# Kernel tuning notes

Hardware: AMD Instinct MI355X
Metric: run time of the kernel (lower is better)

The kernel has to match this reference:

```python
import jax, jax.numpy as jnp
import numpy as np

N = 262144  # num_channels (o*i)
K = 5       # kernel_size


def setup_inputs() -> dict:
    key = jax.random.key(0)
    k1, k2, k3 = jax.random.split(key, 3)
    return {
        "input_filter": jax.random.normal(k1, (N, K, K, K), dtype=jnp.float32),
        "theta_v": jax.random.normal(k2, (N, 3), dtype=jnp.float32),
        "theta": jax.random.normal(k3, (N,), dtype=jnp.float32),
    }


def _rodrigues(theta_v, theta):
    # F.normalize(theta_v, p=2) with eps=1e-12
    norm = jnp.linalg.norm(theta_v, axis=-1, keepdims=True)
    v = theta_v / jnp.maximum(norm, 1e-12)
    vx, vy, vz = v[:, 0], v[:, 1], v[:, 2]
    z = jnp.zeros_like(vx)
    # skew-symmetric cross-product matrix m, shape (n,3,3)
    m = jnp.stack([z, -vz, vy,
                   vz, z, -vx,
                   -vy, vx, z], axis=-1).reshape(-1, 3, 3)
    s = jnp.sin(theta)[:, None, None]
    c = (1.0 - jnp.cos(theta))[:, None, None]
    I3 = jnp.eye(3, dtype=theta_v.dtype)
    return I3 + s * m + c * jnp.einsum('nij,njk->nik', m, m)


def _base_grid(k):
    # matches _get_base_grids: coord along axis i -> channel 0, j -> 1, l -> 2
    c = jnp.linspace(-1.0, 1.0, k, dtype=jnp.float32)
    gi, gj, gl = jnp.meshgrid(c, c, c, indexing='ij')
    return jnp.stack([gi, gj, gl], axis=-1).reshape(k * k * k, 3)  # (k^3, 3)


def _grid_sample_3d_zeros(vol, grid):
    # vol: (n, D, H, W); grid: (n, P, 3) in [-1,1], channels (x->W, y->H, z->D)
    # trilinear, align_corners=True, padding_mode='zeros'
    n, D, H, W = vol.shape
    x = (grid[..., 0] + 1.0) * 0.5 * (W - 1)
    y = (grid[..., 1] + 1.0) * 0.5 * (H - 1)
    z = (grid[..., 2] + 1.0) * 0.5 * (D - 1)
    x0f, y0f, z0f = jnp.floor(x), jnp.floor(y), jnp.floor(z)
    wx, wy, wz = x - x0f, y - y0f, z - z0f
    x0, y0, z0 = x0f.astype(jnp.int32), y0f.astype(jnp.int32), z0f.astype(jnp.int32)
    bidx = jnp.arange(n)[:, None]
    out = jnp.zeros(grid.shape[:-1], dtype=vol.dtype)
    for dz in (0, 1):
        for dy in (0, 1):
            for dx in (0, 1):
                zi, yi, xi = z0 + dz, y0 + dy, x0 + dx
                w = ((wz if dz else 1.0 - wz) *
                     (wy if dy else 1.0 - wy) *
                     (wx if dx else 1.0 - wx))
                inb = ((zi >= 0) & (zi < D) & (yi >= 0) & (yi < H) &
                       (xi >= 0) & (xi < W))
                v = vol[bidx,
                        jnp.clip(zi, 0, D - 1),
                        jnp.clip(yi, 0, H - 1),
                        jnp.clip(xi, 0, W - 1)]
                out = out + w * jnp.where(inb, v, jnp.zeros_like(v))
    return out


def reference(input_filter, theta_v, theta):
    n = theta_v.shape[0]
    k = input_filter.shape[-1]
    vol = input_filter.reshape(n, k, k, k)
    R = _rodrigues(theta_v, theta)                    # (n,3,3)
    base = _base_grid(k)                              # (k^3,3)
    grids = jnp.einsum('pj,njk->npk', base, R)        # (n,k^3,3) = base @ R
    out = _grid_sample_3d_zeros(vol, grids)           # (n,k^3)
    return out.reshape(input_filter.shape)
```

## Files before the change

kernel.cpp:

```cpp
#include <hip/hip_runtime.h>
#include <math.h>

#define KP    125
#define VOL7P 344
#define WPB   4
#define NF    8

typedef _Float16 half_t;
typedef half_t h2 __attribute__((ext_vector_type(2)));
typedef __fp16 fp16x2 __attribute__((ext_vector_type(2)));

static __device__ __forceinline__ h2 h2fma(h2 a, h2 b, h2 c) {
    return __builtin_elementwise_fma(a, b, c);
}
static __device__ __forceinline__ h2 cvt_pk(float a, float b) {
    fp16x2 t = __builtin_amdgcn_cvt_pkrtz(a, b);
    return __builtin_bit_cast(h2, t);
}

__global__ __launch_bounds__(256) void rodrigues_kernel(
    const float* __restrict__ theta_v,
    const float* __restrict__ theta,
    float* __restrict__ Rws, int N)
{
    const int n = blockIdx.x * 256 + threadIdx.x;
    if (n >= N) return;
    const float ax = theta_v[n * 3 + 0];
    const float ay = theta_v[n * 3 + 1];
    const float az = theta_v[n * 3 + 2];
    const float th = theta[n];
    const float d2  = ax * ax + ay * ay + az * az;
    const float inv = rsqrtf(fmaxf(d2, 1e-24f));
    const float vx = ax * inv, vy = ay * inv, vz = az * inv;
    float s, cth;
    __sincosf(th, &s, &cth);
    const float c = 1.0f - cth;
    float4 r0, r1, r2;
    r0.x = 1.0f - c * (vy * vy + vz * vz);
    r0.y = -s * vz + c * (vx * vy);
    r0.z =  s * vy + c * (vx * vz);
    r0.w =  s * vz + c * (vx * vy);
    r1.x = 1.0f - c * (vx * vx + vz * vz);
    r1.y = -s * vx + c * (vy * vz);
    r1.z = -s * vy + c * (vx * vz);
    r1.w =  s * vx + c * (vy * vz);
    r2.x = 1.0f - c * (vx * vx + vy * vy);
    r2.y = 0.f; r2.z = 0.f; r2.w = 0.f;
    float4* o = (float4*)(Rws + (long long)n * 12);
    o[0] = r0; o[1] = r1; o[2] = r2;
}

__global__ __launch_bounds__(WPB * 64) void fastrot_kernel(
    const float* __restrict__ vol,
    const float* __restrict__ Rws,
    float* __restrict__ out)
{
    __shared__ __align__(16) unsigned int pad[WPB][VOL7P];

    const int lane = threadIdx.x & 63;
    const int ws   = __builtin_amdgcn_readfirstlane(threadIdx.x >> 6);
    const long long base = ((long long)blockIdx.x * WPB + ws) * NF;

    uint4* b0 = (uint4*)(&pad[ws][0]);
    const uint4 z4 = make_uint4(0u, 0u, 0u, 0u);
    b0[lane] = z4;
    if (lane < (VOL7P / 4 - 64)) b0[lane + 64] = z4;

    const int p0 = lane, p1 = lane + 64;
    const int i0 = (p0 * 41) >> 10;
    const int q0 = (p0 * 205) >> 10;
    const int j0 = q0 - i0 * 5;
    const int l0 = p0 - q0 * 5;
    const int i1 = (p1 * 41) >> 10;
    const int q1 = (p1 * 205) >> 10;
    const int j1 = q1 - i1 * 5;
    const int l1 = p1 - q1 * 5;
    const bool has1 = (p1 < KP);
    const int e0 = i0 * 49 + j0 * 7 + l0 + 57;
    const int e1 = i1 * 49 + j1 * 7 + l1 + 57;
    const float Bi0 = (float)(i0 - 2), Bj0 = (float)(j0 - 2), Bl0 = (float)(l0 - 2);
    const float Bi1 = (float)(i1 - 2), Bj1 = (float)(j1 - 2), Bl1 = (float)(l1 - 2);

    float fv0[NF], fv1[NF], nx0[NF], nx1[NF];
#pragma unroll
    for (int k = 0; k < NF; ++k) {
        const float* vn = vol + (base + k) * KP;
        fv0[k] = vn[p0];
        fv1[k] = has1 ? vn[p1] : 0.0f;
        nx0[k] = (l0 < 4) ? vn[p0 + 1] : 0.0f;
        nx1[k] = (has1 && l1 < 4) ? vn[p1 + 1] : 0.0f;
    }

    unsigned int* buf = &pad[ws][0];

#pragma unroll
    for (int k = 0; k < NF; ++k) {
        const float* Rp = Rws + (base + k) * 12;
        const float R00 = Rp[0], R01 = Rp[1], R02 = Rp[2];
        const float R10 = Rp[3], R11 = Rp[4], R12 = Rp[5];
        const float R20 = Rp[6], R21 = Rp[7], R22 = Rp[8];

        buf[e0] = __builtin_bit_cast(unsigned int, cvt_pk(fv0[k], nx0[k]));
        if (l0 == 0)
            buf[e0 - 1] = __builtin_bit_cast(unsigned int, cvt_pk(0.0f, fv0[k]));
        if (has1) {
            buf[e1] = __builtin_bit_cast(unsigned int, cvt_pk(fv1[k], nx1[k]));
            if (l1 == 0)
                buf[e1 - 1] = __builtin_bit_cast(unsigned int, cvt_pk(0.0f, fv1[k]));
        }

        float* on = out + (base + k) * KP;

        auto sample = [&](float Bi, float Bj, float Bl) -> float {
            float xf = fmaf(Bi, R00, fmaf(Bj, R10, fmaf(Bl, R20, 3.0f)));
            float yf = fmaf(Bi, R01, fmaf(Bj, R11, fmaf(Bl, R21, 3.0f)));
            float zf = fmaf(Bi, R02, fmaf(Bj, R12, fmaf(Bl, R22, 3.0f)));
            xf = fminf(fmaxf(xf, 0.0f), 5.99993896f);
            yf = fminf(fmaxf(yf, 0.0f), 5.99993896f);
            zf = fminf(fmaxf(zf, 0.0f), 5.99993896f);
            const int x0 = (int)xf, y0 = (int)yf, z0 = (int)zf;
            const float wx = __builtin_amdgcn_fractf(xf);
            const float wy = __builtin_amdgcn_fractf(yf);
            const float wz = __builtin_amdgcn_fractf(zf);
            const int ci = z0 * 49 + y0 * 7 + x0;

            const h2 A0 = __builtin_bit_cast(h2, buf[ci]);
            const h2 A1 = __builtin_bit_cast(h2, buf[ci + 49]);
            const h2 B0 = __builtin_bit_cast(h2, buf[ci + 7]);
            const h2 B1 = __builtin_bit_cast(h2, buf[ci + 56]);

            const h2 wzh = cvt_pk(wz, wz);
            const h2 wyh = cvt_pk(wy, wy);
            const h2 E = h2fma(wzh, A1 - A0, A0);
            const h2 F = h2fma(wzh, B1 - B0, B0);
            const h2 G = h2fma(wyh, F - E, E);
            const float g0 = (float)G.x;
            const float g1 = (float)G.y;
            return fmaf(wx, g1 - g0, g0);
        };

        on[p0] = sample(Bi0, Bj0, Bl0);
        if (has1) on[p1] = sample(Bi1, Bj1, Bl1);
    }
}

__global__ __launch_bounds__(512) void fastrot_fb_kernel(
    const float* __restrict__ vol,
    const float* __restrict__ theta_v,
    const float* __restrict__ theta,
    float* __restrict__ out)
{
    __shared__ __align__(16) float pad[8][344];
    __shared__ float sR[8][12];

    const int lane = threadIdx.x & 63;
    const int wv   = threadIdx.x >> 6;
    const long long nb = (long long)blockIdx.x * 8;
    const long long n  = nb + wv;

    float4* p4 = (float4*)(&pad[wv][0]);
    const float4 z4 = make_float4(0.f, 0.f, 0.f, 0.f);
    p4[lane] = z4;
    if (lane < (344 / 4 - 64)) p4[lane + 64] = z4;

    const float* vn = vol + n * (long long)KP;
    const int p0 = lane, p1 = lane + 64;
    const float fv0 = vn[p0];
    const float fv1 = (p1 < KP) ? vn[p1] : 0.0f;

    const int i0 = (p0 * 41) >> 10;
    const int q0 = (p0 * 205) >> 10;
    const int j0 = q0 - i0 * 5;
    const int l0 = p0 - q0 * 5;
    const int i1 = (p1 * 41) >> 10;
    const int q1 = (p1 * 205) >> 10;
    const int j1 = q1 - i1 * 5;
    const int l1 = p1 - q1 * 5;

    pad[wv][i0 * 49 + j0 * 7 + l0 + 57] = fv0;
    if (p1 < KP) pad[wv][i1 * 49 + j1 * 7 + l1 + 57] = fv1;

    if (wv == 0 && lane < 8) {
        const long long m = nb + lane;
        const float ax = theta_v[m * 3 + 0];
        const float ay = theta_v[m * 3 + 1];
        const float az = theta_v[m * 3 + 2];
        const float th = theta[m];
        const float d2  = ax * ax + ay * ay + az * az;
        const float inv = rsqrtf(fmaxf(d2, 1e-24f));
        const float vx = ax * inv, vy = ay * inv, vz = az * inv;
        float s, cth;
        __sincosf(th, &s, &cth);
        const float c = 1.0f - cth;
        float* R = &sR[lane][0];
        R[0] = 1.0f - c * (vy * vy + vz * vz);
        R[1] = -s * vz + c * (vx * vy);
        R[2] =  s * vy + c * (vx * vz);
        R[3] =  s * vz + c * (vx * vy);
        R[4] = 1.0f - c * (vx * vx + vz * vz);
        R[5] = -s * vx + c * (vy * vz);
        R[6] = -s * vy + c * (vx * vz);
        R[7] =  s * vx + c * (vy * vz);
        R[8] = 1.0f - c * (vx * vx + vy * vy);
    }

    __syncthreads();

    const float R00 = sR[wv][0], R01 = sR[wv][1], R02 = sR[wv][2];
    const float R10 = sR[wv][3], R11 = sR[wv][4], R12 = sR[wv][5];
    const float R20 = sR[wv][6], R21 = sR[wv][7], R22 = sR[wv][8];

    const float* pw = &pad[wv][0];
    float* on = out + n * (long long)KP;

    auto sample = [&](float Bi, float Bj, float Bl) -> float {
        float xf = fmaf(Bi, R00, fmaf(Bj, R10, fmaf(Bl, R20, 3.0f)));
        float yf = fmaf(Bi, R01, fmaf(Bj, R11, fmaf(Bl, R21, 3.0f)));
        float zf = fmaf(Bi, R02, fmaf(Bj, R12, fmaf(Bl, R22, 3.0f)));
        xf = fminf(fmaxf(xf, 0.0f), 5.99993896f);
        yf = fminf(fmaxf(yf, 0.0f), 5.99993896f);
        zf = fminf(fmaxf(zf, 0.0f), 5.99993896f);
        const int x0 = (int)xf, y0 = (int)yf, z0 = (int)zf;
        const float wx = __builtin_amdgcn_fractf(xf);
        const float wy = __builtin_amdgcn_fractf(yf);
        const float wz = __builtin_amdgcn_fractf(zf);
        const int ci = z0 * 49 + y0 * 7 + x0;
        const float a00 = pw[ci],      a01 = pw[ci + 1];
        const float a10 = pw[ci + 7],  a11 = pw[ci + 8];
        const float a20 = pw[ci + 49], a21 = pw[ci + 50];
        const float a30 = pw[ci + 56], a31 = pw[ci + 57];
        const float r0 = fmaf(wx, a01 - a00, a00);
        const float r1 = fmaf(wx, a11 - a10, a10);
        const float r2 = fmaf(wx, a21 - a20, a20);
        const float r3 = fmaf(wx, a31 - a30, a30);
        const float s0 = fmaf(wy, r1 - r0, r0);
        const float s1 = fmaf(wy, r3 - r2, r2);
        return fmaf(wz, s1 - s0, s0);
    };

    on[p0] = sample((float)(i0 - 2), (float)(j0 - 2), (float)(l0 - 2));
    if (p1 < KP)
        on[p1] = sample((float)(i1 - 2), (float)(j1 - 2), (float)(l1 - 2));
}

extern "C" void kernel_launch(void* const* d_in, const int* in_sizes, int n_in,
                              void* d_out, int out_size, void* d_ws, size_t ws_size,
                              hipStream_t stream) {
    const float* vol     = (const float*)d_in[0];
    const float* theta_v = (const float*)d_in[1];
    const float* theta   = (const float*)d_in[2];
    float* out           = (float*)d_out;

    const int N = in_sizes[2];

    const size_t need = (size_t)N * 12 * sizeof(float);
    if (ws_size >= need) {
        float* Rws = (float*)d_ws;
        rodrigues_kernel<<<(N + 255) / 256, 256, 0, stream>>>(theta_v, theta, Rws, N);
        fastrot_kernel<<<N / (WPB * NF), WPB * 64, 0, stream>>>(vol, Rws, out);
    } else {
        fastrot_fb_kernel<<<N / 8, 512, 0, stream>>>(vol, theta_v, theta, out);
    }
}
```

Measured before the change: 61.76 us.

## Fuse Rodrigues rotation computation into sampling kernel via lane broadcast

Removes the separate rodrigues_kernel and its workspace round trip. Each wavefront now computes the rotation matrices for its 8 filters in lanes 0-7 and broadcasts them with readlane inside the per-filter loop. The fallback kernel and workspace branch are deleted. This saves a kernel launch and the global write and read of 12 floats per filter, at the cost of redundant trig work in each wave (lanes 8-63 duplicate it) and some extra scalar readlane instructions.

```diff
diff --git a/kernel.cpp b/kernel.cpp
--- a/kernel.cpp
+++ b/kernel.cpp
@@ -17,42 +17,15 @@
     fp16x2 t = __builtin_amdgcn_cvt_pkrtz(a, b);
     return __builtin_bit_cast(h2, t);
 }
-
-__global__ __launch_bounds__(256) void rodrigues_kernel(
-    const float* __restrict__ theta_v,
-    const float* __restrict__ theta,
-    float* __restrict__ Rws, int N)
-{
-    const int n = blockIdx.x * 256 + threadIdx.x;
-    if (n >= N) return;
-    const float ax = theta_v[n * 3 + 0];
-    const float ay = theta_v[n * 3 + 1];
-    const float az = theta_v[n * 3 + 2];
-    const float th = theta[n];
-    const float d2  = ax * ax + ay * ay + az * az;
-    const float inv = rsqrtf(fmaxf(d2, 1e-24f));
-    const float vx = ax * inv, vy = ay * inv, vz = az * inv;
-    float s, cth;
-    __sincosf(th, &s, &cth);
-    const float c = 1.0f - cth;
-    float4 r0, r1, r2;
-    r0.x = 1.0f - c * (vy * vy + vz * vz);
-    r0.y = -s * vz + c * (vx * vy);
-    r0.z =  s * vy + c * (vx * vz);
-    r0.w =  s * vz + c * (vx * vy);
-    r1.x = 1.0f - c * (vx * vx + vz * vz);
-    r1.y = -s * vx + c * (vy * vz);
-    r1.z = -s * vy + c * (vx * vz);
-    r1.w =  s * vx + c * (vy * vz);
-    r2.x = 1.0f - c * (vx * vx + vy * vy);
-    r2.y = 0.f; r2.z = 0.f; r2.w = 0.f;
-    float4* o = (float4*)(Rws + (long long)n * 12);
-    o[0] = r0; o[1] = r1; o[2] = r2;
+static __device__ __forceinline__ float rdlane(float v, int k) {
+    return __builtin_bit_cast(float,
+        __builtin_amdgcn_readlane(__builtin_bit_cast(int, v), k));
 }
 
 __global__ __launch_bounds__(WPB * 64) void fastrot_kernel(
     const float* __restrict__ vol,
-    const float* __restrict__ Rws,
+    const float* __restrict__ theta_v,
+    const float* __restrict__ theta,
     float* __restrict__ out)
 {
     __shared__ __align__(16) unsigned int pad[WPB][VOL7P];
@@ -65,6 +38,30 @@
     const uint4 z4 = make_uint4(0u, 0u, 0u, 0u);
     b0[lane] = z4;
     if (lane < (VOL7P / 4 - 64)) b0[lane + 64] = z4;
+
+    float r00, r01, r02, r10, r11, r12, r20, r21, r22;
+    {
+        const long long m = base + (lane & (NF - 1));
+        const float ax = theta_v[m * 3 + 0];
+        const float ay = theta_v[m * 3 + 1];
+        const float az = theta_v[m * 3 + 2];
+        const float th = theta[m];
+        const float d2  = ax * ax + ay * ay + az * az;
+        const float inv = rsqrtf(fmaxf(d2, 1e-24f));
+        const float vx = ax * inv, vy = ay * inv, vz = az * inv;
+        float s, cth;
+        __sincosf(th, &s, &cth);
+        const float c = 1.0f - cth;
+        r00 = 1.0f - c * (vy * vy + vz * vz);
+        r01 = -s * vz + c * (vx * vy);
+        r02 =  s * vy + c * (vx * vz);
+        r10 =  s * vz + c * (vx * vy);
+        r11 = 1.0f - c * (vx * vx + vz * vz);
+        r12 = -s * vx + c * (vy * vz);
+        r20 = -s * vy + c * (vx * vz);
+        r21 =  s * vx + c * (vy * vz);
+        r22 = 1.0f - c * (vx * vx + vy * vy);
+    }
 
     const int p0 = lane, p1 = lane + 64;
     const int i0 = (p0 * 41) >> 10;
@@ -95,10 +92,9 @@
 
 #pragma unroll
     for (int k = 0; k < NF; ++k) {
-        const float* Rp = Rws + (base + k) * 12;
-        const float R00 = Rp[0], R01 = Rp[1], R02 = Rp[2];
-        const float R10 = Rp[3], R11 = Rp[4], R12 = Rp[5];
-        const float R20 = Rp[6], R21 = Rp[7], R22 = Rp[8];
+        const float R00 = rdlane(r00, k), R01 = rdlane(r01, k), R02 = rdlane(r02, k);
+        const float R10 = rdlane(r10, k), R11 = rdlane(r11, k), R12 = rdlane(r12, k);
+        const float R20 = rdlane(r20, k), R21 = rdlane(r21, k), R22 = rdlane(r22, k);
 
         buf[e0] = __builtin_bit_cast(unsigned int, cvt_pk(fv0[k], nx0[k]));
         if (l0 == 0)
@@ -144,105 +140,6 @@
     }
 }
 
-__global__ __launch_bounds__(512) void fastrot_fb_kernel(
-    const float* __restrict__ vol,
-    const float* __restrict__ theta_v,
-    const float* __restrict__ theta,
-    float* __restrict__ out)
-{
-    __shared__ __align__(16) float pad[8][344];
-    __shared__ float sR[8][12];
-
-    const int lane = threadIdx.x & 63;
-    const int wv   = threadIdx.x >> 6;
-    const long long nb = (long long)blockIdx.x * 8;
-    const long long n  = nb + wv;
-
-    float4* p4 = (float4*)(&pad[wv][0]);
-    const float4 z4 = make_float4(0.f, 0.f, 0.f, 0.f);
-    p4[lane] = z4;
-    if (lane < (344 / 4 - 64)) p4[lane + 64] = z4;
-
-    const float* vn = vol + n * (long long)KP;
-    const int p0 = lane, p1 = lane + 64;
-    const float fv0 = vn[p0];
-    const float fv1 = (p1 < KP) ? vn[p1] : 0.0f;
-
-    const int i0 = (p0 * 41) >> 10;
-    const int q0 = (p0 * 205) >> 10;
-    const int j0 = q0 - i0 * 5;
-    const int l0 = p0 - q0 * 5;
-    const int i1 = (p1 * 41) >> 10;
-    const int q1 = (p1 * 205) >> 10;
-    const int j1 = q1 - i1 * 5;
-    const int l1 = p1 - q1 * 5;
-
-    pad[wv][i0 * 49 + j0 * 7 + l0 + 57] = fv0;
-    if (p1 < KP) pad[wv][i1 * 49 + j1 * 7 + l1 + 57] = fv1;
-
-    if (wv == 0 && lane < 8) {
-        const long long m = nb + lane;
-        const float ax = theta_v[m * 3 + 0];
-        const float ay = theta_v[m * 3 + 1];
-        const float az = theta_v[m * 3 + 2];
-        const float th = theta[m];
-        const float d2  = ax * ax + ay * ay + az * az;
-        const float inv = rsqrtf(fmaxf(d2, 1e-24f));
-        const float vx = ax * inv, vy = ay * inv, vz = az * inv;
-        float s, cth;
-        __sincosf(th, &s, &cth);
-        const float c = 1.0f - cth;
-        float* R = &sR[lane][0];
-        R[0] = 1.0f - c * (vy * vy + vz * vz);
-        R[1] = -s * vz + c * (vx * vy);
-        R[2] =  s * vy + c * (vx * vz);
-        R[3] =  s * vz + c * (vx * vy);
-        R[4] = 1.0f - c * (vx * vx + vz * vz);
-        R[5] = -s * vx + c * (vy * vz);
-        R[6] = -s * vy + c * (vx * vz);
-        R[7] =  s * vx + c * (vy * vz);
-        R[8] = 1.0f - c * (vx * vx + vy * vy);
-    }
-
-    __syncthreads();
-
-    const float R00 = sR[wv][0], R01 = sR[wv][1], R02 = sR[wv][2];
-    const float R10 = sR[wv][3], R11 = sR[wv][4], R12 = sR[wv][5];
-    const float R20 = sR[wv][6], R21 = sR[wv][7], R22 = sR[wv][8];
-
-    const float* pw = &pad[wv][0];
-    float* on = out + n * (long long)KP;
-
-    auto sample = [&](float Bi, float Bj, float Bl) -> float {
-        float xf = fmaf(Bi, R00, fmaf(Bj, R10, fmaf(Bl, R20, 3.0f)));
-        float yf = fmaf(Bi, R01, fmaf(Bj, R11, fmaf(Bl, R21, 3.0f)));
-        float zf = fmaf(Bi, R02, fmaf(Bj, R12, fmaf(Bl, R22, 3.0f)));
-        xf = fminf(fmaxf(xf, 0.0f), 5.99993896f);
-        yf = fminf(fmaxf(yf, 0.0f), 5.99993896f);
-        zf = fminf(fmaxf(zf, 0.0f), 5.99993896f);
-        const int x0 = (int)xf, y0 = (int)yf, z0 = (int)zf;
-        const float wx = __builtin_amdgcn_fractf(xf);
-        const float wy = __builtin_amdgcn_fractf(yf);
-        const float wz = __builtin_amdgcn_fractf(zf);
-        const int ci = z0 * 49 + y0 * 7 + x0;
-        const float a00 = pw[ci],      a01 = pw[ci + 1];
-        const float a10 = pw[ci + 7],  a11 = pw[ci + 8];
-        const float a20 = pw[ci + 49], a21 = pw[ci + 50];
-        const float a30 = pw[ci + 56], a31 = pw[ci + 57];
-        const float r0 = fmaf(wx, a01 - a00, a00);
-        const float r1 = fmaf(wx, a11 - a10, a10);
-        const float r2 = fmaf(wx, a21 - a20, a20);
-        const float r3 = fmaf(wx, a31 - a30, a30);
-        const float s0 = fmaf(wy, r1 - r0, r0);
-        const float s1 = fmaf(wy, r3 - r2, r2);
-        return fmaf(wz, s1 - s0, s0);
-    };
-
-    on[p0] = sample((float)(i0 - 2), (float)(j0 - 2), (float)(l0 - 2));
-    if (p1 < KP)
-        on[p1] = sample((float)(i1 - 2), (float)(j1 - 2), (float)(l1 - 2));
-}
-
 extern "C" void kernel_launch(void* const* d_in, const int* in_sizes, int n_in,
                               void* d_out, int out_size, void* d_ws, size_t ws_size,
                               hipStream_t stream) {
@@ -253,12 +150,5 @@
 
     const int N = in_sizes[2];
 
-    const size_t need = (size_t)N * 12 * sizeof(float);
-    if (ws_size >= need) {
-        float* Rws = (float*)d_ws;
-        rodrigues_kernel<<<(N + 255) / 256, 256, 0, stream>>>(theta_v, theta, Rws, N);
-        fastrot_kernel<<<N / (WPB * NF), WPB * 64, 0, stream>>>(vol, Rws, out);
-    } else {
-        fastrot_fb_kernel<<<N / 8, 512, 0, stream>>>(vol, theta_v, theta, out);
-    }
+    fastrot_kernel<<<N / (WPB * NF), WPB * 64, 0, stream>>>(vol, theta_v, theta, out);
 }
```

Result: faster. 56.37 us (-8.7%).
